# Kernel tuning notes

Hardware: AMD Instinct MI355X
Metric: run time of the kernel (lower is better)

## Reference

```python
import jax, jax.numpy as jnp
import numpy as np

T, B, D, H, O = 64, 64, 512, 512, 128

def setup_inputs() -> dict:
    key = jax.random.key(0)
    ks = jax.random.split(key, 8)
    s = 0.05
    return {
        "x": jax.random.normal(ks[0], (T, B, D), jnp.float32),
        "w_ih": jax.random.normal(ks[1], (T, 4 * H, D), jnp.float32) * s,
        "w_hh": jax.random.normal(ks[2], (T, 4 * H, H), jnp.float32) * s,
        "b_ih": jax.random.normal(ks[3], (T, 4 * H), jnp.float32) * s,
        "b_hh": jax.random.normal(ks[4], (T, 4 * H), jnp.float32) * s,
        "w_ho": jax.random.normal(ks[5], (O, H), jnp.float32) * s,
        "b_ho": jax.random.normal(ks[6], (O,), jnp.float32) * s,
        "lengths": jax.random.randint(ks[7], (B,), 1, T + 1, jnp.int64 if jax.config.jax_enable_x64 else jnp.int32),
    }

def _lstm_scan(x, w_ih, w_hh, b_ih, b_hh):
    bs = x.shape[1]
    h0 = jnp.zeros((bs, H), x.dtype)
    c0 = jnp.zeros((bs, H), x.dtype)

    def step(carry, inp):
        h, c = carry
        xt, Wih, Whh, bih, bhh = inp
        # gates: [B, 4H], torch gate order i, f, g, o
        gates = xt @ Wih.T + bih + h @ Whh.T + bhh
        i, f, g, o = jnp.split(gates, 4, axis=-1)
        c = jax.nn.sigmoid(f) * c + jax.nn.sigmoid(i) * jnp.tanh(g)
        h = jax.nn.sigmoid(o) * jnp.tanh(c)
        return (h, c), h

    (_, _), outs = jax.lax.scan(step, (h0, c0), (x, w_ih, w_hh, b_ih, b_hh))
    return outs  # [T, B, H]

def reference(x, w_ih, w_hh, b_ih, b_hh, w_ho, b_ho, lengths):
    outs = _lstm_scan(x, w_ih, w_hh, b_ih, b_hh)
    bs = x.shape[1]
    h_t = outs[lengths - 1, jnp.arange(bs)]  # [B, H] last valid output per seq
    logits = h_t @ w_ho.T + b_ho
    return jax.nn.log_softmax(logits, axis=1)
```

## Files before the change

### kernel.cpp

```cpp
#include <hip/hip_runtime.h>
#include <math.h>

#define TT 64
#define BB 64
#define DD 512
#define HH 512
#define G4 2048
#define OO 128

typedef unsigned short us16;
typedef __attribute__((ext_vector_type(8))) short bf16x8;
typedef __attribute__((ext_vector_type(4))) float f32x4;
typedef __attribute__((ext_vector_type(4))) unsigned u32x4;

__device__ __forceinline__ unsigned pk_bf16(float lo, float hi) {
  unsigned r;
  asm volatile("v_cvt_pk_bf16_f32 %0, %1, %2" : "=v"(r) : "v"(lo), "v"(hi));
  return r;
}

__device__ __forceinline__ float fsigm(float v) { return 1.f / (1.f + __expf(-v)); }
__device__ __forceinline__ float ftanh(float v) { return 1.f - 2.f / (__expf(2.f * v) + 1.f); }

__device__ __forceinline__ u32x4 load_b128_cc(const void* p) {
  u32x4 r;
  asm volatile("global_load_dwordx4 %0, %1, off sc0 sc1" : "=v"(r) : "v"(p));
  return r;
}
__device__ __forceinline__ void store_b32u_cc(void* p, unsigned v) {
  asm volatile("global_store_dword %0, %1, off sc0 sc1" ::"v"(p), "v"(v) : "memory");
}

__global__ __launch_bounds__(256) void phaseA_mfma(
    const float* __restrict__ x, const float* __restrict__ wih,
    const float* __restrict__ bih, const float* __restrict__ bhh,
    float* __restrict__ Gb) {
  __shared__ us16 xa[2][64][64];
  __shared__ us16 wbuf[2][128][64];
  const int tid = threadIdx.x;
  const int t = blockIdx.y;
  const int j0 = blockIdx.x * 128;
  const int wv = tid >> 6, lane = tid & 63;
  const int wm = wv & 1, wn = wv >> 1;
  const float* xb = x + (size_t)t * (BB * DD);
  const float* wg = wih + (size_t)t * (G4 * DD) + (size_t)j0 * DD;

  float4 xr[2][2], wr[4][2];
  int xrow[2], xc[2], wrow[4], wc[4];
#pragma unroll
  for (int i = 0; i < 2; i++) { int cid = tid + i * 256; xrow[i] = cid >> 3; xc[i] = cid & 7; }
#pragma unroll
  for (int i = 0; i < 4; i++) { int cid = tid + i * 256; wrow[i] = cid >> 3; wc[i] = cid & 7; }

  auto loadx = [&](int k0) {
#pragma unroll
    for (int i = 0; i < 2; i++) {
      const float* p = xb + xrow[i] * DD + k0 + xc[i] * 8;
      xr[i][0] = *(const float4*)p; xr[i][1] = *(const float4*)(p + 4);
    }
  };
  auto loadw = [&](int k0) {
#pragma unroll
    for (int i = 0; i < 4; i++) {
      const float* p = wg + (size_t)wrow[i] * DD + k0 + wc[i] * 8;
      wr[i][0] = *(const float4*)p; wr[i][1] = *(const float4*)(p + 4);
    }
  };
  auto store = [&](int buf) {
#pragma unroll
    for (int i = 0; i < 2; i++) {
      uint4 u;
      u.x = pk_bf16(xr[i][0].x, xr[i][0].y); u.y = pk_bf16(xr[i][0].z, xr[i][0].w);
      u.z = pk_bf16(xr[i][1].x, xr[i][1].y); u.w = pk_bf16(xr[i][1].z, xr[i][1].w);
      int p = xc[i] ^ (xrow[i] & 7);
      *(uint4*)&xa[buf][xrow[i]][p * 8] = u;
    }
#pragma unroll
    for (int i = 0; i < 4; i++) {
      uint4 u;
      u.x = pk_bf16(wr[i][0].x, wr[i][0].y); u.y = pk_bf16(wr[i][0].z, wr[i][0].w);
      u.z = pk_bf16(wr[i][1].x, wr[i][1].y); u.w = pk_bf16(wr[i][1].z, wr[i][1].w);
      int p = wc[i] ^ (wrow[i] & 7);
      *(uint4*)&wbuf[buf][wrow[i]][p * 8] = u;
    }
  };

  loadx(0); loadw(0); store(0);
  __syncthreads();

  f32x4 zero = {0.f, 0.f, 0.f, 0.f};
  f32x4 acc[2][4];
#pragma unroll
  for (int mt = 0; mt < 2; mt++)
#pragma unroll
    for (int nt = 0; nt < 4; nt++) acc[mt][nt] = zero;

  for (int s = 0; s < 8; s++) {
    const int nb = s & 1;
    if (s < 7) { loadx((s + 1) * 64); loadw((s + 1) * 64); }
#pragma unroll
    for (int ks = 0; ks < 2; ks++) {
      const int cc = ks * 4 + (lane >> 4);
      bf16x8 a[2], b[4];
#pragma unroll
      for (int mt = 0; mt < 2; mt++) {
        int r = wm * 32 + mt * 16 + (lane & 15);
        a[mt] = *(const bf16x8*)&xa[nb][r][(cc ^ (r & 7)) * 8];
      }
#pragma unroll
      for (int nt = 0; nt < 4; nt++) {
        int r = wn * 64 + nt * 16 + (lane & 15);
        b[nt] = *(const bf16x8*)&wbuf[nb][r][(cc ^ (r & 7)) * 8];
      }
#pragma unroll
      for (int mt = 0; mt < 2; mt++)
#pragma unroll
        for (int nt = 0; nt < 4; nt++)
          acc[mt][nt] = __builtin_amdgcn_mfma_f32_16x16x32_bf16(a[mt], b[nt], acc[mt][nt], 0, 0, 0);
    }
    __syncthreads();
    if (s < 7) store(nb ^ 1);
    __syncthreads();
  }

  float bias[4]; int jn[4];
#pragma unroll
  for (int nt = 0; nt < 4; nt++) {
    jn[nt] = j0 + wn * 64 + nt * 16 + (lane & 15);
    bias[nt] = bih[t * G4 + jn[nt]] + bhh[t * G4 + jn[nt]];
  }
#pragma unroll
  for (int mt = 0; mt < 2; mt++)
#pragma unroll
    for (int nt = 0; nt < 4; nt++)
#pragma unroll
      for (int e = 0; e < 4; e++) {
        int brow = wm * 32 + mt * 16 + (lane >> 4) * 4 + e;
        Gb[((size_t)t * BB + brow) * G4 + jn[nt]] = acc[mt][nt][e] + bias[nt];
      }
}

__global__ __launch_bounds__(256, 1) void lstm_persist(
    const float* __restrict__ whh, const float* __restrict__ Gb,
    const int* __restrict__ lengths, char* __restrict__ hb,
    float* __restrict__ hf) {
  __shared__ float gm[2][16][36];

  const int tid = threadIdx.x, bid = blockIdx.x;
  const int bh = bid & 1, ug = bid >> 1;
  const int wv = tid >> 6, lane = tid & 63;
  const int wm = wv & 1, kq = wv >> 1;
  const int l15 = lane & 15, klg = lane >> 4;
  const unsigned M = 0x40004000u;

  const size_t jrow = (size_t)((l15 >> 2) * 512 + ug * 4 + (l15 & 3));

  float4 pf[8][2];
  auto prefW = [&](int tt) {
    const float* wt = whh + (size_t)tt * (G4 * HH) + jrow * HH;
#pragma unroll
    for (int s = 0; s < 8; s++) {
      const float* p = wt + (size_t)(kq * 32 + s * 4 + klg) * 8;
      pf[s][0] = *(const float4*)p;
      pf[s][1] = *(const float4*)(p + 4);
    }
  };
  bf16x8 wfrag[8];
  auto cvtW = [&]() {
#pragma unroll
    for (int s = 0; s < 8; s++) {
      uint4 u;
      u.x = pk_bf16(pf[s][0].x, pf[s][0].y); u.y = pk_bf16(pf[s][0].z, pf[s][0].w);
      u.z = pk_bf16(pf[s][1].x, pf[s][1].y); u.w = pk_bf16(pf[s][1].z, pf[s][1].w);
      wfrag[s] = __builtin_bit_cast(bf16x8, u);
    }
  };

  float2 gpre[4];
  auto prefG = [&](int tt) {
    if (wv == 0) {
      const float* gbp =
          Gb + ((size_t)tt * BB + bh * 32 + (lane & 31)) * G4 + ug * 4 + ((lane >> 5) << 1);
#pragma unroll
      for (int q = 0; q < 4; q++) gpre[q] = *(const float2*)(gbp + q * 512);
    }
  };

  const size_t cbase =
      (size_t)bh * 32768 + ((size_t)(kq * 32 + klg) * 32 + wm * 16 + l15) * 16;
  const size_t pbase = (size_t)bh * 32768 +
                       ((size_t)(ug >> 1) * 32 + (lane & 31)) * 16 +
                       (size_t)((ug * 2 + (lane >> 5)) & 3) * 4;

  const int mylen = (wv == 0) ? lengths[bh * 32 + (lane & 31)] : -2;
  float cst[2] = {0.f, 0.f};

  prefW(0);
  prefG(0);

  for (int t = 0; t < TT; t++) {
    cvtW();

    u32x4 r[8];
    if (t == 0) {
      u32x4 z = {0u, 0u, 0u, 0u};
#pragma unroll
      for (int s = 0; s < 8; s++) r[s] = z;
    } else {
      const char* sbase = hb + (size_t)(t & 1) * 65536 + cbase;
      const unsigned tw = ((t >> 1) & 1) ? M : 0u;
      bool ok;
      do {
#pragma unroll
        for (int s = 0; s < 8; s++) r[s] = load_b128_cc(sbase + (size_t)s * 2048);
        asm volatile("s_waitcnt vmcnt(0)" ::: "memory");
        __builtin_amdgcn_sched_barrier(0);
        unsigned bad = 0u;
#pragma unroll
        for (int s = 0; s < 8; s++) {
          bad |= ((r[s].x & M) ^ tw) | ((r[s].y & M) ^ tw);
          bad |= ((r[s].z & M) ^ tw) | ((r[s].w & M) ^ tw);
        }
        if (!__all(bad == 0u)) {
          __builtin_amdgcn_s_sleep(1);
          ok = false;
        } else {
          ok = true;
        }
      } while (!ok);
#pragma unroll
      for (int s = 0; s < 8; s++) r[s] &= 0xBFFFBFFFu;
    }

    f32x4 acc = {0.f, 0.f, 0.f, 0.f};
#pragma unroll
    for (int s = 0; s < 8; s++)
      acc = __builtin_amdgcn_mfma_f32_16x16x32_bf16(__builtin_bit_cast(bf16x8, r[s]),
                                                    wfrag[s], acc, 0, 0, 0);
    *(f32x4*)&gm[kq][l15][wm * 16 + klg * 4] = acc;

    __syncthreads();

    float2 gcur[4];
    if (wv == 0) {
#pragma unroll
      for (int q = 0; q < 4; q++) gcur[q] = gpre[q];
    }
    if (t + 1 < TT) { prefW(t + 1); prefG(t + 1); }

    if (wv == 0) {
      const int b = lane & 31, hi = lane >> 5;
      float hv[2];
#pragma unroll
      for (int uu = 0; uu < 2; uu++) {
        const int lu = hi * 2 + uu;
        float vi = (uu ? gcur[0].y : gcur[0].x) + gm[0][0 + lu][b] + gm[1][0 + lu][b];
        float vf = (uu ? gcur[1].y : gcur[1].x) + gm[0][4 + lu][b] + gm[1][4 + lu][b];
        float vg = (uu ? gcur[2].y : gcur[2].x) + gm[0][8 + lu][b] + gm[1][8 + lu][b];
        float vo = (uu ? gcur[3].y : gcur[3].x) + gm[0][12 + lu][b] + gm[1][12 + lu][b];
        float cn = fsigm(vf) * cst[uu] + fsigm(vi) * ftanh(vg);
        cst[uu] = cn;
        hv[uu] = fsigm(vo) * ftanh(cn);
      }
      if (t + 1 < TT) {
        unsigned tagb = (((t + 1) >> 1) & 1) ? M : 0u;
        unsigned hw = pk_bf16(hv[0], hv[1]) | tagb;
        store_b32u_cc(hb + (size_t)((t + 1) & 1) * 65536 + pbase, hw);
      }
      if (mylen - 1 == t) {
        float2 o2; o2.x = hv[0]; o2.y = hv[1];
        *(float2*)&hf[(size_t)(bh * 32 + b) * HH + ug * 4 + hi * 2] = o2;
      }
    }
  }
}

__global__ __launch_bounds__(128) void finalK(const float* __restrict__ hf,
                                              const float* __restrict__ who,
                                              const float* __restrict__ bho,
                                              float* __restrict__ out) {
  int b = blockIdx.x, o = threadIdx.x;
  const float* h = hf + b * HH;
  const float* w = who + o * HH;
  float s = bho[o];
#pragma unroll 4
  for (int k = 0; k < HH; k += 4) {
    float4 hv = *(const float4*)(h + k);
    float4 wv = *(const float4*)(w + k);
    s += hv.x * wv.x + hv.y * wv.y + hv.z * wv.z + hv.w * wv.w;
  }
  __shared__ float red[2];
  __shared__ float red2[2];
  float m = s;
#pragma unroll
  for (int msk = 32; msk; msk >>= 1) m = fmaxf(m, __shfl_xor(m, msk));
  int wave = o >> 6;
  if ((o & 63) == 0) red[wave] = m;
  __syncthreads();
  m = fmaxf(red[0], red[1]);
  float e = expf(s - m);
#pragma unroll
  for (int msk = 32; msk; msk >>= 1) e += __shfl_xor(e, msk);
  if ((o & 63) == 0) red2[wave] = e;
  __syncthreads();
  float sum = red2[0] + red2[1];
  out[b * OO + o] = (s - m) - logf(sum);
}

extern "C" void kernel_launch(void* const* d_in, const int* in_sizes, int n_in,
                              void* d_out, int out_size, void* d_ws, size_t ws_size,
                              hipStream_t stream) {
  const float* x = (const float*)d_in[0];
  const float* wih = (const float*)d_in[1];
  const float* whh = (const float*)d_in[2];
  const float* bih = (const float*)d_in[3];
  const float* bhh = (const float*)d_in[4];
  const float* who = (const float*)d_in[5];
  const float* bho = (const float*)d_in[6];
  const int* lengths = (const int*)d_in[7];
  float* out = (float*)d_out;

  char* ws = (char*)d_ws;
  float* Gb = (float*)ws;
  char* hb = ws + 33554432;
  float* hf = (float*)(ws + 33554432 + 131072);

  (void)hipMemsetAsync(hb, 0x00, 65536, stream);
  (void)hipMemsetAsync(hb + 65536, 0x40, 65536, stream);

  phaseA_mfma<<<dim3(16, 64), 256, 0, stream>>>(x, wih, bih, bhh, Gb);
  lstm_persist<<<256, 256, 0, stream>>>(whh, Gb, lengths, hb, hf);
  finalK<<<BB, 128, 0, stream>>>(hf, who, bho, out);
}
```

Baseline: 376.6 us.

## Halve persistent LSTM grid by giving each block eight hidden units

```diff
diff --git a/kernel.cpp b/kernel.cpp
--- a/kernel.cpp
+++ b/kernel.cpp
@@ -12,6 +12,7 @@
 typedef __attribute__((ext_vector_type(8))) short bf16x8;
 typedef __attribute__((ext_vector_type(4))) float f32x4;
 typedef __attribute__((ext_vector_type(4))) unsigned u32x4;
+typedef __attribute__((ext_vector_type(2))) unsigned u32x2;
 
 __device__ __forceinline__ unsigned pk_bf16(float lo, float hi) {
   unsigned r;
@@ -27,8 +28,8 @@
   asm volatile("global_load_dwordx4 %0, %1, off sc0 sc1" : "=v"(r) : "v"(p));
   return r;
 }
-__device__ __forceinline__ void store_b32u_cc(void* p, unsigned v) {
-  asm volatile("global_store_dword %0, %1, off sc0 sc1" ::"v"(p), "v"(v) : "memory");
+__device__ __forceinline__ void store_b64_cc(void* p, u32x2 v) {
+  asm volatile("global_store_dwordx2 %0, %1, off sc0 sc1" ::"v"(p), "v"(v) : "memory");
 }
 
 __global__ __launch_bounds__(256) void phaseA_mfma(
@@ -144,56 +145,68 @@
     const float* __restrict__ whh, const float* __restrict__ Gb,
     const int* __restrict__ lengths, char* __restrict__ hb,
     float* __restrict__ hf) {
-  __shared__ float gm[2][16][36];
+  __shared__ float gm[2][32][36];
 
   const int tid = threadIdx.x, bid = blockIdx.x;
-  const int bh = bid & 1, ug = bid >> 1;
+  const int bh = bid & 1, u8 = bid >> 1;
   const int wv = tid >> 6, lane = tid & 63;
   const int wm = wv & 1, kq = wv >> 1;
   const int l15 = lane & 15, klg = lane >> 4;
   const unsigned M = 0x40004000u;
 
-  const size_t jrow = (size_t)((l15 >> 2) * 512 + ug * 4 + (l15 & 3));
-
-  float4 pf[8][2];
+  size_t jrow[2];
+#pragma unroll
+  for (int n = 0; n < 2; n++) {
+    int ri = n * 16 + l15;
+    jrow[n] = (size_t)((ri >> 3) * 512 + u8 * 8 + (ri & 7));
+  }
+
+  float4 pf[2][8][2];
   auto prefW = [&](int tt) {
-    const float* wt = whh + (size_t)tt * (G4 * HH) + jrow * HH;
-#pragma unroll
-    for (int s = 0; s < 8; s++) {
-      const float* p = wt + (size_t)(kq * 32 + s * 4 + klg) * 8;
-      pf[s][0] = *(const float4*)p;
-      pf[s][1] = *(const float4*)(p + 4);
-    }
-  };
-  bf16x8 wfrag[8];
+    const float* wt = whh + (size_t)tt * (G4 * HH);
+#pragma unroll
+    for (int n = 0; n < 2; n++) {
+      const float* wr = wt + jrow[n] * HH;
+#pragma unroll
+      for (int s = 0; s < 8; s++) {
+        const float* p = wr + (size_t)(kq * 32 + s * 4 + klg) * 8;
+        pf[n][s][0] = *(const float4*)p;
+        pf[n][s][1] = *(const float4*)(p + 4);
+      }
+    }
+  };
+  bf16x8 wfrag[2][8];
   auto cvtW = [&]() {
 #pragma unroll
-    for (int s = 0; s < 8; s++) {
-      uint4 u;
-      u.x = pk_bf16(pf[s][0].x, pf[s][0].y); u.y = pk_bf16(pf[s][0].z, pf[s][0].w);
-      u.z = pk_bf16(pf[s][1].x, pf[s][1].y); u.w = pk_bf16(pf[s][1].z, pf[s][1].w);
-      wfrag[s] = __builtin_bit_cast(bf16x8, u);
-    }
-  };
-
-  float2 gpre[4];
+    for (int n = 0; n < 2; n++)
+#pragma unroll
+      for (int s = 0; s < 8; s++) {
+        uint4 u;
+        u.x = pk_bf16(pf[n][s][0].x, pf[n][s][0].y);
+        u.y = pk_bf16(pf[n][s][0].z, pf[n][s][0].w);
+        u.z = pk_bf16(pf[n][s][1].x, pf[n][s][1].y);
+        u.w = pk_bf16(pf[n][s][1].z, pf[n][s][1].w);
+        wfrag[n][s] = __builtin_bit_cast(bf16x8, u);
+      }
+  };
+
+  f32x4 gpre[4];
   auto prefG = [&](int tt) {
     if (wv == 0) {
-      const float* gbp =
-          Gb + ((size_t)tt * BB + bh * 32 + (lane & 31)) * G4 + ug * 4 + ((lane >> 5) << 1);
-#pragma unroll
-      for (int q = 0; q < 4; q++) gpre[q] = *(const float2*)(gbp + q * 512);
+      const float* gbp = Gb + ((size_t)tt * BB + bh * 32 + (lane & 31)) * G4 +
+                         u8 * 8 + (lane >> 5) * 4;
+#pragma unroll
+      for (int q = 0; q < 4; q++) gpre[q] = *(const f32x4*)(gbp + q * 512);
     }
   };
 
   const size_t cbase =
       (size_t)bh * 32768 + ((size_t)(kq * 32 + klg) * 32 + wm * 16 + l15) * 16;
-  const size_t pbase = (size_t)bh * 32768 +
-                       ((size_t)(ug >> 1) * 32 + (lane & 31)) * 16 +
-                       (size_t)((ug * 2 + (lane >> 5)) & 3) * 4;
+  const size_t pbase =
+      (size_t)bh * 32768 + ((size_t)u8 * 32 + (lane & 31)) * 16 + (size_t)(lane >> 5) * 8;
 
   const int mylen = (wv == 0) ? lengths[bh * 32 + (lane & 31)] : -2;
-  float cst[2] = {0.f, 0.f};
+  float cst[4] = {0.f, 0.f, 0.f, 0.f};
 
   prefW(0);
   prefG(0);
@@ -232,16 +245,19 @@
       for (int s = 0; s < 8; s++) r[s] &= 0xBFFFBFFFu;
     }
 
-    f32x4 acc = {0.f, 0.f, 0.f, 0.f};
-#pragma unroll
-    for (int s = 0; s < 8; s++)
-      acc = __builtin_amdgcn_mfma_f32_16x16x32_bf16(__builtin_bit_cast(bf16x8, r[s]),
-                                                    wfrag[s], acc, 0, 0, 0);
-    *(f32x4*)&gm[kq][l15][wm * 16 + klg * 4] = acc;
+    f32x4 acc0 = {0.f, 0.f, 0.f, 0.f}, acc1 = {0.f, 0.f, 0.f, 0.f};
+#pragma unroll
+    for (int s = 0; s < 8; s++) {
+      bf16x8 a = __builtin_bit_cast(bf16x8, r[s]);
+      acc0 = __builtin_amdgcn_mfma_f32_16x16x32_bf16(a, wfrag[0][s], acc0, 0, 0, 0);
+      acc1 = __builtin_amdgcn_mfma_f32_16x16x32_bf16(a, wfrag[1][s], acc1, 0, 0, 0);
+    }
+    *(f32x4*)&gm[kq][l15][wm * 16 + klg * 4] = acc0;
+    *(f32x4*)&gm[kq][16 + l15][wm * 16 + klg * 4] = acc1;
 
     __syncthreads();
 
-    float2 gcur[4];
+    f32x4 gcur[4];
     if (wv == 0) {
 #pragma unroll
       for (int q = 0; q < 4; q++) gcur[q] = gpre[q];
@@ -250,26 +266,28 @@
 
     if (wv == 0) {
       const int b = lane & 31, hi = lane >> 5;
-      float hv[2];
-#pragma unroll
-      for (int uu = 0; uu < 2; uu++) {
-        const int lu = hi * 2 + uu;
-        float vi = (uu ? gcur[0].y : gcur[0].x) + gm[0][0 + lu][b] + gm[1][0 + lu][b];
-        float vf = (uu ? gcur[1].y : gcur[1].x) + gm[0][4 + lu][b] + gm[1][4 + lu][b];
-        float vg = (uu ? gcur[2].y : gcur[2].x) + gm[0][8 + lu][b] + gm[1][8 + lu][b];
-        float vo = (uu ? gcur[3].y : gcur[3].x) + gm[0][12 + lu][b] + gm[1][12 + lu][b];
+      float hv[4];
+#pragma unroll
+      for (int uu = 0; uu < 4; uu++) {
+        const int u = hi * 4 + uu;
+        float vi = gcur[0][uu] + gm[0][0 + u][b] + gm[1][0 + u][b];
+        float vf = gcur[1][uu] + gm[0][8 + u][b] + gm[1][8 + u][b];
+        float vg = gcur[2][uu] + gm[0][16 + u][b] + gm[1][16 + u][b];
+        float vo = gcur[3][uu] + gm[0][24 + u][b] + gm[1][24 + u][b];
         float cn = fsigm(vf) * cst[uu] + fsigm(vi) * ftanh(vg);
         cst[uu] = cn;
         hv[uu] = fsigm(vo) * ftanh(cn);
       }
       if (t + 1 < TT) {
-        unsigned tagb = (((t + 1) >> 1) & 1) ? M : 0u;
-        unsigned hw = pk_bf16(hv[0], hv[1]) | tagb;
-        store_b32u_cc(hb + (size_t)((t + 1) & 1) * 65536 + pbase, hw);
+        const unsigned tagb = (((t + 1) >> 1) & 1) ? M : 0u;
+        u32x2 rec;
+        rec.x = pk_bf16(hv[0], hv[1]) | tagb;
+        rec.y = pk_bf16(hv[2], hv[3]) | tagb;
+        store_b64_cc(hb + (size_t)((t + 1) & 1) * 65536 + pbase, rec);
       }
       if (mylen - 1 == t) {
-        float2 o2; o2.x = hv[0]; o2.y = hv[1];
-        *(float2*)&hf[(size_t)(bh * 32 + b) * HH + ug * 4 + hi * 2] = o2;
+        f32x4 o = {hv[0], hv[1], hv[2], hv[3]};
+        *(f32x4*)&hf[(size_t)(bh * 32 + b) * HH + u8 * 8 + hi * 4] = o;
       }
     }
   }
@@ -329,6 +347,6 @@
   (void)hipMemsetAsync(hb + 65536, 0x40, 65536, stream);
 
   phaseA_mfma<<<dim3(16, 64), 256, 0, stream>>>(x, wih, bih, bhh, Gb);
-  lstm_persist<<<256, 256, 0, stream>>>(whh, Gb, lengths, hb, hf);
+  lstm_persist<<<128, 256, 0, stream>>>(whh, Gb, lengths, hb, hf);
   finalK<<<BB, 128, 0, stream>>>(hf, who, bho, out);
 }
```

New measurement: 531.2 us. 1.41x slower.
